# Optimization experiments

Hardware: AMD Instinct MI355X
Metric: run time of the kernel (lower is better)

## Reference

```python
import jax, jax.numpy as jnp
import numpy as np
from jax import lax

B, N, S, NS = 32, 2048, 256, 16   # batch, seeds, proposals (must be 16*16), ball-query samples
C_IN = 256                         # seed_feat_dim
RADIUS = 0.3
EPS = 1e-5
NAB, NVP = 12, 12                  # num_angle_bin, num_viewpoint
GROUPS, PLANES = 4, 64             # SpatialCGNL groups / bottleneck planes
C_OUT = 2 + 3 + 1 + 1 + 2 * NAB + NVP  # 43


def fps(xyz, npoint):
    """Furthest point sampling (torch pointnet2 style: start at index 0)."""
    Bb, Nn, _ = xyz.shape
    def step(carry, _):
        dist, far = carry
        cen = jnp.take_along_axis(xyz, far[:, None, None], axis=1)      # (B,1,3)
        d = jnp.sum((xyz - cen) ** 2, axis=-1)                          # (B,N)
        dist = jnp.minimum(dist, d)
        return (dist, jnp.argmax(dist, axis=1).astype(jnp.int32)), far
    init = (jnp.full((Bb, Nn), 1e10, xyz.dtype), jnp.zeros((Bb,), jnp.int32))
    _, inds = lax.scan(step, init, None, length=npoint)
    return jnp.transpose(inds)  # (B,npoint)


def ball_query(xyz, new_xyz, radius, nsample):
    """First-nsample neighbors within radius; pad by duplicating the first hit."""
    d2 = jnp.sum((new_xyz[:, :, None, :] - xyz[:, None, :, :]) ** 2, axis=-1)  # (B,S,N)
    Nn = xyz.shape[1]
    cand = jnp.where(d2 < radius * radius, jnp.arange(Nn)[None, None, :], Nn)
    idx = jnp.sort(cand, axis=-1)[..., :nsample]
    idx = jnp.where(idx == Nn, idx[..., :1], idx)   # duplicate first hit
    idx = jnp.where(idx == Nn, 0, idx)              # no neighbor at all -> 0
    return idx


def bn1d(x, g, b, m, v):
    """Inference BatchNorm1d over channel axis of (B,C,S)."""
    s = (g * lax.rsqrt(v + EPS))
    return (x - m[None, :, None]) * s[None, :, None] + b[None, :, None]


def forward(xyz, features, sa_w0, sa_w1, sa_w2, sa_gamma, sa_beta, sa_mean, sa_var,
            wt, wp, wg, wz, gn_gamma, gn_beta,
            c1_w, c1_b, bn1_g, bn1_b, bn1_m, bn1_v,
            c2_w, c2_b, bn2_g, bn2_b, bn2_m, bn2_v, c3_w, c3_b):
    # ---- PointnetSAModuleVotes (vote_fps sampling) ----
    fps_inds = fps(xyz, S)                                               # (B,S)
    new_xyz = jnp.take_along_axis(xyz, fps_inds[:, :, None], axis=1)     # (B,S,3)
    idx = ball_query(xyz, new_xyz, RADIUS, NS)                           # (B,S,NS)
    gather = jax.vmap(lambda a, i: a[i])
    g_xyz = (gather(xyz, idx) - new_xyz[:, :, None, :]) / RADIUS         # (B,S,NS,3), normalize_xyz
    g_feat = gather(jnp.transpose(features, (0, 2, 1)), idx)             # (B,S,NS,C)
    h = jnp.concatenate([g_xyz, g_feat], axis=-1)                        # (B,S,NS,3+C)
    for i, w in enumerate((sa_w0, sa_w1, sa_w2)):                        # SharedMLP: conv1x1(no bias)+BN+ReLU
        h = jnp.einsum('bsnc,oc->bsno', h, w)
        h = jax.nn.relu((h - sa_mean[i]) * (sa_gamma[i] * lax.rsqrt(sa_var[i] + EPS)) + sa_beta[i])
    x = jnp.transpose(jnp.max(h, axis=2), (0, 2, 1))                     # max-pool over NS -> (B,128,S)

    # ---- SpatialCGNL (use_scale=False, groups=4), spatial 16x16 flattened to S ----
    t = jnp.einsum('oc,bcn->bon', wt, x)                                 # (B,64,S)
    p = jnp.einsum('oc,bcn->bon', wp, x)
    g = jnp.einsum('oc,bcn->bon', wg, x)
    cg = PLANES // GROUPS                                                # 16
    tg = t.reshape(B, GROUPS, cg * S)
    pg = p.reshape(B, GROUPS, cg * S)
    gg = g.reshape(B, GROUPS, cg * S)
    att = jnp.sum(pg * gg, axis=-1, keepdims=True)                       # (B,G,1) scalar per group
    y = (att * tg).reshape(B, GROUPS, cg, S)                             # (B,G,16,S)
    wz_g = wz.reshape(GROUPS, 128 // GROUPS, cg)                         # grouped 1x1 conv 64->128
    y = jnp.einsum('goc,bgcn->bgon', wz_g, y).reshape(B, 128, S)
    # GroupNorm(num_groups=4, num_channels=128)
    yg = y.reshape(B, GROUPS, -1)
    mu = jnp.mean(yg, axis=-1, keepdims=True)
    var = jnp.mean((yg - mu) ** 2, axis=-1, keepdims=True)
    yn = ((yg - mu) * lax.rsqrt(var + EPS)).reshape(B, 128, S)
    y = yn * gn_gamma[None, :, None] + gn_beta[None, :, None] + x        # affine + residual

    # ---- conv/bn/relu head ----
    h1 = jax.nn.relu(bn1d(jnp.einsum('oc,bcn->bon', c1_w, y) + c1_b[None, :, None], bn1_g, bn1_b, bn1_m, bn1_v))
    h2 = jax.nn.relu(bn1d(jnp.einsum('oc,bcn->bon', c2_w, h1) + c2_b[None, :, None], bn2_g, bn2_b, bn2_m, bn2_v))
    net = jnp.einsum('oc,bcn->bon', c3_w, h2) + c3_b[None, :, None]      # (B,43,S)

    # ---- decode_scores ----
    nt = jnp.transpose(net, (0, 2, 1))                                   # (B,S,43)
    center = new_xyz + nt[:, :, 2:5]
    ang_res_n = nt[:, :, 7 + NAB:7 + 2 * NAB]
    out = jnp.concatenate([
        nt[:, :, 0:2],                    # objectness_scores
        center,                           # center
        nt[:, :, 5:7 + 2 * NAB],          # width, quality, angle_scores, angle_residuals_normalized
        ang_res_n * jnp.float32(np.pi / NAB),  # angle_residuals
        nt[:, :, 7 + 2 * NAB:],           # viewpoint_scores
    ], axis=-1)                           # (B,S,55)
    return out


def setup_inputs():
    key = jax.random.key(0)
    ks = iter(jax.random.split(key, 32))
    rn = lambda shape, s=0.05: jax.random.normal(next(ks), shape, jnp.float32) * s
    return dict(
        xyz=rn((B, N, 3), 1.0),
        features=rn((B, C_IN, N), 1.0),
        sa_w0=rn((128, C_IN + 3)), sa_w1=rn((128, 128)), sa_w2=rn((128, 128)),
        sa_gamma=jnp.ones((3, 128)), sa_beta=jnp.zeros((3, 128)),
        sa_mean=jnp.zeros((3, 128)), sa_var=jnp.ones((3, 128)),
        wt=rn((PLANES, 128)), wp=rn((PLANES, 128)), wg=rn((PLANES, 128)),
        wz=rn((128, PLANES // GROUPS)),
        gn_gamma=jnp.ones((128,)), gn_beta=jnp.zeros((128,)),
        c1_w=rn((128, 128)), c1_b=jnp.zeros((128,)),
        bn1_g=jnp.ones((128,)), bn1_b=jnp.zeros((128,)), bn1_m=jnp.zeros((128,)), bn1_v=jnp.ones((128,)),
        c2_w=rn((128, 128)), c2_b=jnp.zeros((128,)),
        bn2_g=jnp.ones((128,)), bn2_b=jnp.zeros((128,)), bn2_m=jnp.zeros((128,)), bn2_v=jnp.ones((128,)),
        c3_w=rn((C_OUT, 128)), c3_b=jnp.zeros((C_OUT,)),
    )


def reference(xyz, features, sa_w0, sa_w1, sa_w2, sa_gamma, sa_beta, sa_mean, sa_var,
              wt, wp, wg, wz, gn_gamma, gn_beta,
              c1_w, c1_b, bn1_g, bn1_b, bn1_m, bn1_v,
              c2_w, c2_b, bn2_g, bn2_b, bn2_m, bn2_v, c3_w, c3_b):
    return forward(xyz, features, sa_w0, sa_w1, sa_w2, sa_gamma, sa_beta, sa_mean, sa_var,
                   wt, wp, wg, wz, gn_gamma, gn_beta,
                   c1_w, c1_b, bn1_g, bn1_b, bn1_m, bn1_v,
                   c2_w, c2_b, bn2_g, bn2_b, bn2_m, bn2_v, c3_w, c3_b)
```

## Files before the change

### kernel.cpp

```cpp
#include <hip/hip_runtime.h>
#include <hip/hip_bf16.h>
#include <math.h>

#define Bx   32
#define Nx   2048
#define Sx   256
#define NSx  16
#define CINx 256

typedef unsigned short u16;
typedef unsigned int   u32;
typedef unsigned long long u64;
typedef short bf16x8 __attribute__((ext_vector_type(8)));
typedef float f32x4  __attribute__((ext_vector_type(4)));

__device__ __forceinline__ float b2f(u16 u) {
  union { u32 i; float f; } v; v.i = ((u32)u) << 16; return v.f;
}
__device__ __forceinline__ u16 f2b(float x) {
  u32 u = __float_as_uint(x);
  u32 r = (u + 0x7FFFu + ((u >> 16) & 1u)) >> 16;
  return (u16)r;
}
__device__ __forceinline__ float ldin(const void* p, size_t i, int bf) {
  return bf ? b2f(((const u16*)p)[i]) : ((const float*)p)[i];
}

#define DPP_FMAX(x, ctrl)                                                      \
  x = fmaxf(x, __int_as_float(__builtin_amdgcn_update_dpp(                     \
          __float_as_int(x), __float_as_int(x), (ctrl), 0xf, 0xf, false)))

#define OFF_FEATT 0
#define OFF_XT    (33554432)
#define OFF_T     (OFF_XT + 4194304)
#define OFF_YT    (OFF_T + 2097152)
#define OFF_NXYZ  (OFF_YT + 4194304)
#define OFF_IDX   (OFF_NXYZ + 98304)
#define OFF_ATT   (OFF_IDX + 524288)
#define OFF_W0F   (OFF_ATT + 512)
#define OFF_B0    (OFF_W0F + 133120)
#define OFF_W1F   (OFF_B0 + 512)
#define OFF_B1    (OFF_W1F + 65536)
#define OFF_W2F   (OFF_B1 + 512)
#define OFF_B2    (OFF_W2F + 65536)
#define OFF_WTT   (OFF_B2 + 512)
#define OFF_WPT   (OFF_WTT + 32768)
#define OFF_WGT   (OFF_WPT + 32768)
#define OFF_C1T   (OFF_WGT + 32768)
#define OFF_D1    (OFF_C1T + 65536)
#define OFF_C2T   (OFF_D1 + 512)
#define OFF_D2    (OFF_C2T + 65536)
#define OFF_C3T   (OFF_D2 + 512)
#define OFF_WZF   (OFF_C3T + 22016)
#define OFF_GNG   (OFF_WZF + 8192)
#define OFF_GNB   (OFF_GNG + 512)
#define OFF_C3B   (OFF_GNB + 512)
#define OFF_FLAG  (OFF_C3B + 512)

__global__ __launch_bounds__(256) void k_sniff(const u32* __restrict__ w, int* __restrict__ flag) {
  __shared__ int cnt;
  int t = threadIdx.x;
  if (t == 0) cnt = 0;
  __syncthreads();
  u32 x = w[t];
  int e_lo = (x >> 7) & 0xFF;
  if (e_lo >= 100 && e_lo <= 140) atomicAdd(&cnt, 1);
  __syncthreads();
  if (t == 0) *flag = (cnt > 128) ? 1 : 0;
}

#define TRANS_BLKS 4096
__global__ __launch_bounds__(256) void k_mega(
    const void* __restrict__ xyzR, const void* __restrict__ featR,
    const void* sa_w0, const void* sa_w1, const void* sa_w2,
    const void* sa_g,  const void* sa_b,  const void* sa_m, const void* sa_v,
    const void* wt, const void* wp, const void* wg, const void* wzI,
    const void* gngI, const void* gnbI,
    const void* c1w, const void* c1b,
    const void* bn1g, const void* bn1b, const void* bn1m, const void* bn1v,
    const void* c2w, const void* c2b,
    const void* bn2g, const void* bn2b, const void* bn2m, const void* bn2v,
    const void* c3w, const void* c3bI,
    float* __restrict__ nxyz, u16* __restrict__ featT,
    u16* __restrict__ w0F, float* __restrict__ b0, u16* __restrict__ w1F, float* __restrict__ b1,
    u16* __restrict__ w2F, float* __restrict__ b2,
    float* __restrict__ wtT, float* __restrict__ wpT, float* __restrict__ wgT,
    float* __restrict__ c1T, float* __restrict__ d1, float* __restrict__ c2T, float* __restrict__ d2,
    float* __restrict__ c3T, float* __restrict__ wzF, float* __restrict__ gngF,
    float* __restrict__ gnbF, float* __restrict__ c3bF,
    const int* __restrict__ flagp) {
  __shared__ union {
    struct { float sxyz[Nx * 3]; u64 red[2][4]; } fps;
    u16 tile[64][65];
  } sm;
  int bid = blockIdx.x, t = threadIdx.x;
  int bf = *flagp;

  if (bid < Bx) {
    int b = bid;
    const size_t xb = (size_t)b * Nx * 3;
    for (int i = t; i < Nx * 3; i += 256) sm.fps.sxyz[i] = ldin(xyzR, xb + i, bf);
    __syncthreads();
    float px[8], py[8], pz[8], dist[8];
#pragma unroll
    for (int j = 0; j < 8; ++j) {
      int p = t * 8 + j;
      px[j] = sm.fps.sxyz[p * 3 + 0];
      py[j] = sm.fps.sxyz[p * 3 + 1];
      pz[j] = sm.fps.sxyz[p * 3 + 2];
      dist[j] = 1e10f;
    }
    int lane = t & 63, w = t >> 6;
    int far = 0, myind = 0;
    for (int it = 0; it < Sx; ++it) {
      if (t == it) myind = far;
      float cx = sm.fps.sxyz[far * 3 + 0];
      float cy = sm.fps.sxyz[far * 3 + 1];
      float cz = sm.fps.sxyz[far * 3 + 2];
      float bv = -1.f; int bj = 0;
#pragma unroll
      for (int j = 0; j < 8; ++j) {
        float dx = __fsub_rn(px[j], cx);
        float dy = __fsub_rn(py[j], cy);
        float dz = __fsub_rn(pz[j], cz);
        float d = __fadd_rn(__fadd_rn(__fmul_rn(dx, dx), __fmul_rn(dy, dy)), __fmul_rn(dz, dz));
        float nd = fminf(dist[j], d);
        dist[j] = nd;
        if (nd > bv) { bv = nd; bj = j; }
      }
      int bi = t * 8 + bj;
      float x = bv;
      DPP_FMAX(x, 0x111);
      DPP_FMAX(x, 0x112);
      DPP_FMAX(x, 0x114);
      DPP_FMAX(x, 0x118);
      DPP_FMAX(x, 0x142);
      DPP_FMAX(x, 0x143);
      float wmax = __int_as_float(__builtin_amdgcn_readlane(__float_as_int(x), 63));
      u64 mk = __ballot(bv == wmax);
      int srcl = (int)__builtin_ctzll(mk);
      int wbi = __builtin_amdgcn_readlane(bi, srcl);
      if (lane == 63)
        sm.fps.red[it & 1][w] = ((u64)__float_as_uint(wmax) << 32) | (u32)(~wbi);
      __syncthreads();
      u64 k0 = sm.fps.red[it & 1][0], k1 = sm.fps.red[it & 1][1];
      u64 k2 = sm.fps.red[it & 1][2], k3 = sm.fps.red[it & 1][3];
      u64 best = k0 > k1 ? k0 : k1;
      if (k2 > best) best = k2;
      if (k3 > best) best = k3;
      far = (int)(u32)(~(u32)best);
    }
    float* o = nxyz + ((size_t)b * Sx + t) * 3;
    o[0] = sm.fps.sxyz[myind * 3 + 0];
    o[1] = sm.fps.sxyz[myind * 3 + 1];
    o[2] = sm.fps.sxyz[myind * 3 + 2];
  } else if (bid < Bx + TRANS_BLKS) {
    int tb = bid - Bx;
    int nblk = tb & 31, rest = tb >> 5;
    int cblk = rest & 3, b = rest >> 2;
    int n0 = nblk * 64, c0 = cblk * 64;
    int tx = t & 63, ty = t >> 6;
#pragma unroll
    for (int r = ty; r < 64; r += 4) {
      size_t src = ((size_t)(b * CINx + c0 + r)) * Nx + n0 + tx;
      sm.tile[r][tx] = bf ? ((const u16*)featR)[src] : f2b(((const float*)featR)[src]);
    }
    __syncthreads();
#pragma unroll
    for (int r = ty; r < 64; r += 4)
      featT[((size_t)(b * Nx + n0 + r)) * CINx + c0 + tx] = sm.tile[tx][r];
  } else {
    int g0 = (bid - Bx - TRANS_BLKS) * 256 + t;
    const int gs = 64 * 256;
    for (int i = g0; i < 9 * 8 * 64 * 8; i += gs) {
      int j = i & 7, lane = (i >> 3) & 63, nt = (i >> 9) & 7, kt = i >> 12;
      int o = nt * 16 + (lane & 15);
      int c = kt * 32 + (lane >> 4) * 8 + j;
      float s = ldin(sa_g, o, bf) * rsqrtf(ldin(sa_v, o, bf) + 1e-5f);
      float w;
      if (c < 256) w = ldin(sa_w0, o * 259 + 3 + c, bf);
      else if (c < 259) w = ldin(sa_w0, o * 259 + (c - 256), bf);
      else w = 0.f;
      w0F[i] = f2b(w * s);
    }
    for (int i = g0; i < 4 * 8 * 64 * 8; i += gs) {
      int j = i & 7, lane = (i >> 3) & 63, nt = (i >> 9) & 7, kt = i >> 12;
      int o = nt * 16 + (lane & 15);
      int c = kt * 32 + (lane >> 4) * 8 + j;
      float s1 = ldin(sa_g, 128 + o, bf) * rsqrtf(ldin(sa_v, 128 + o, bf) + 1e-5f);
      float s2 = ldin(sa_g, 256 + o, bf) * rsqrtf(ldin(sa_v, 256 + o, bf) + 1e-5f);
      w1F[i] = f2b(ldin(sa_w1, o * 128 + c, bf) * s1);
      w2F[i] = f2b(ldin(sa_w2, o * 128 + c, bf) * s2);
    }
    for (int o = g0; o < 128; o += gs) {
      float s0 = ldin(sa_g, o, bf)       * rsqrtf(ldin(sa_v, o, bf)       + 1e-5f);
      float s1 = ldin(sa_g, 128 + o, bf) * rsqrtf(ldin(sa_v, 128 + o, bf) + 1e-5f);
      float s2 = ldin(sa_g, 256 + o, bf) * rsqrtf(ldin(sa_v, 256 + o, bf) + 1e-5f);
      b0[o] = ldin(sa_b, o, bf)       - ldin(sa_m, o, bf)       * s0;
      b1[o] = ldin(sa_b, 128 + o, bf) - ldin(sa_m, 128 + o, bf) * s1;
      b2[o] = ldin(sa_b, 256 + o, bf) - ldin(sa_m, 256 + o, bf) * s2;
      float sc1 = ldin(bn1g, o, bf) * rsqrtf(ldin(bn1v, o, bf) + 1e-5f);
      float sc2 = ldin(bn2g, o, bf) * rsqrtf(ldin(bn2v, o, bf) + 1e-5f);
      d1[o] = (ldin(c1b, o, bf) - ldin(bn1m, o, bf)) * sc1 + ldin(bn1b, o, bf);
      d2[o] = (ldin(c2b, o, bf) - ldin(bn2m, o, bf)) * sc2 + ldin(bn2b, o, bf);
      gngF[o] = ldin(gngI, o, bf);
      gnbF[o] = ldin(gnbI, o, bf);
    }
    for (int i = g0; i < 128 * 128; i += gs) {
      int o = i >> 7, c = i & 127;
      float sc1 = ldin(bn1g, o, bf) * rsqrtf(ldin(bn1v, o, bf) + 1e-5f);
      float sc2 = ldin(bn2g, o, bf) * rsqrtf(ldin(bn2v, o, bf) + 1e-5f);
      c1T[c * 128 + o] = ldin(c1w, i, bf) * sc1;
      c2T[c * 128 + o] = ldin(c2w, i, bf) * sc2;
    }
    for (int i = g0; i < 64 * 128; i += gs) {
      int o = i >> 7, c = i & 127;
      wtT[c * 64 + o] = ldin(wt, i, bf);
      wpT[c * 64 + o] = ldin(wp, i, bf);
      wgT[c * 64 + o] = ldin(wg, i, bf);
    }
    for (int i = g0; i < 43 * 128; i += gs) {
      int o = i >> 7, c = i & 127;
      c3T[c * 43 + o] = ldin(c3w, i, bf);
    }
    for (int i = g0; i < 2048; i += gs) wzF[i] = ldin(wzI, i, bf);
    for (int i = g0; i < 43; i += gs) c3bF[i] = ldin(c3bI, i, bf);
  }
}

__global__ __launch_bounds__(256) void k_ballq(const void* __restrict__ xyzR,
                                               const float* __restrict__ nxyz,
                                               int* __restrict__ idxb,
                                               const int* __restrict__ flagp) {
  int bf = *flagp;
  int t = threadIdx.x;
  int wv = t >> 6, lane = t & 63;
  int gs = blockIdx.x * 4 + wv;
  int b = gs >> 8;
  const size_t xb = (size_t)b * Nx * 3;
  const float* cen = nxyz + (size_t)gs * 3;
  float cx = cen[0], cy = cen[1], cz = cen[2];
  const float R2 = (float)(0.3 * 0.3);
  int* outp = idxb + (size_t)gs * NSx;
  int have = 0, first = 0;
  bool gotfirst = false;
  for (int ch = 0; ch < Nx / 64 && have < NSx; ++ch) {
    int p = ch * 64 + lane;
    float dx = __fsub_rn(ldin(xyzR, xb + p * 3 + 0, bf), cx);
    float dy = __fsub_rn(ldin(xyzR, xb + p * 3 + 1, bf), cy);
    float dz = __fsub_rn(ldin(xyzR, xb + p * 3 + 2, bf), cz);
    float d2 = __fadd_rn(__fadd_rn(__fmul_rn(dx, dx), __fmul_rn(dy, dy)), __fmul_rn(dz, dz));
    bool hit = d2 < R2;
    unsigned long long m = __ballot(hit);
    if (hit) {
      int pos = have + __popcll(m & ((1ull << lane) - 1ull));
      if (pos < NSx) outp[pos] = p;
    }
    if (!gotfirst && m) { first = ch * 64 + (int)__builtin_ctzll(m); gotfirst = true; }
    have += __popcll(m);
  }
  if (have < NSx && lane >= have && lane < NSx) outp[lane] = first;
}

__global__ __launch_bounds__(256) void k_samlp(
    const u16* __restrict__ featT, const void* __restrict__ xyzR,
    const float* __restrict__ nxyz, const int* __restrict__ idxb,
    const u16* __restrict__ w0F, const float* __restrict__ b0v,
    const u16* __restrict__ w1F, const float* __restrict__ b1v,
    const u16* __restrict__ w2F, const float* __restrict__ b2v,
    float* __restrict__ xT, const int* __restrict__ flagp) {
  __shared__ __align__(16) u16 lds[4][16 * 32 + 2 * 16 * 136];
  int bf = *flagp;
  int t = threadIdx.x, w = t >> 6, lane = t & 63;
  int s = blockIdx.x * 4 + w, b = blockIdx.y;
  u16* ht = &lds[w][0];
  u16* hA = &lds[w][512];
  u16* hB = &lds[w][512 + 2176];
  const int* gidx = idxb + ((size_t)b * Sx + s) * NSx;
  int m = lane & 15, q = lane >> 4;
  int pn = gidx[m];
  const float* cen = nxyz + ((size_t)b * Sx + s) * 3;
  for (int i = lane; i < 16 * 32; i += 64)
    if ((i & 31) >= 3) ht[i] = 0;
  if (lane < 48) {
    int n2 = lane / 3, cc = lane - n2 * 3;
    int pn2 = gidx[n2];
    float v = (ldin(xyzR, ((size_t)b * Nx + pn2) * 3 + cc, bf) - cen[cc]) * (1.0f / 0.3f);
    ht[n2 * 32 + cc] = f2b(v);
  }
  __syncthreads();

  const bf16x8* wf0 = (const bf16x8*)w0F;
  const bf16x8* wf1 = (const bf16x8*)w1F;
  const bf16x8* wf2 = (const bf16x8*)w2F;
  f32x4 acc[8];

#pragma unroll
  for (int nt = 0; nt < 8; ++nt) acc[nt] = (f32x4){0.f, 0.f, 0.f, 0.f};
  const u16* arow = featT + ((size_t)b * Nx + pn) * CINx + q * 8;
#pragma unroll
  for (int kt = 0; kt < 9; ++kt) {
    bf16x8 a = (kt < 8) ? *(const bf16x8*)(arow + kt * 32)
                        : *(const bf16x8*)(ht + m * 32 + q * 8);
#pragma unroll
    for (int nt = 0; nt < 8; ++nt)
      acc[nt] = __builtin_amdgcn_mfma_f32_16x16x32_bf16(a, wf0[(kt * 8 + nt) * 64 + lane], acc[nt], 0, 0, 0);
  }
#pragma unroll
  for (int nt = 0; nt < 8; ++nt) {
    float bb = b0v[nt * 16 + m];
#pragma unroll
    for (int r = 0; r < 4; ++r)
      hA[(q * 4 + r) * 136 + nt * 16 + m] = f2b(fmaxf(acc[nt][r] + bb, 0.f));
  }
  __syncthreads();

#pragma unroll
  for (int nt = 0; nt < 8; ++nt) acc[nt] = (f32x4){0.f, 0.f, 0.f, 0.f};
#pragma unroll
  for (int kt = 0; kt < 4; ++kt) {
    bf16x8 a = *(const bf16x8*)(hA + m * 136 + kt * 32 + q * 8);
#pragma unroll
    for (int nt = 0; nt < 8; ++nt)
      acc[nt] = __builtin_amdgcn_mfma_f32_16x16x32_bf16(a, wf1[(kt * 8 + nt) * 64 + lane], acc[nt], 0, 0, 0);
  }
#pragma unroll
  for (int nt = 0; nt < 8; ++nt) {
    float bb = b1v[nt * 16 + m];
#pragma unroll
    for (int r = 0; r < 4; ++r)
      hB[(q * 4 + r) * 136 + nt * 16 + m] = f2b(fmaxf(acc[nt][r] + bb, 0.f));
  }
  __syncthreads();

#pragma unroll
  for (int nt = 0; nt < 8; ++nt) acc[nt] = (f32x4){0.f, 0.f, 0.f, 0.f};
#pragma unroll
  for (int kt = 0; kt < 4; ++kt) {
    bf16x8 a = *(const bf16x8*)(hB + m * 136 + kt * 32 + q * 8);
#pragma unroll
    for (int nt = 0; nt < 8; ++nt)
      acc[nt] = __builtin_amdgcn_mfma_f32_16x16x32_bf16(a, wf2[(kt * 8 + nt) * 64 + lane], acc[nt], 0, 0, 0);
  }
  float* xrow = xT + ((size_t)b * Sx + s) * 128;
#pragma unroll
  for (int nt = 0; nt < 8; ++nt) {
    float vm = fmaxf(fmaxf(acc[nt][0], acc[nt][1]), fmaxf(acc[nt][2], acc[nt][3]));
    vm = fmaxf(vm, __shfl_xor(vm, 16, 64));
    vm = fmaxf(vm, __shfl_xor(vm, 32, 64));
    float v = fmaxf(vm + b2v[nt * 16 + m], 0.f);
    if (q == 0) xrow[nt * 16 + m] = v;
  }
}

__global__ __launch_bounds__(256) void k_tpg(const float* __restrict__ xT,
                                             const float* __restrict__ wtT,
                                             const float* __restrict__ wpT,
                                             const float* __restrict__ wgT,
                                             float* __restrict__ tbuf,
                                             float* __restrict__ att) {
  __shared__ float xs[64][129];
  int b = blockIdx.y, s0 = blockIdx.x * 64, t = threadIdx.x;
  {
    int r = t >> 2, part = (t & 3) * 32;
    const float4* src = (const float4*)(xT + ((size_t)b * Sx + s0 + r) * 128 + part);
#pragma unroll
    for (int q = 0; q < 8; ++q) {
      float4 v = src[q];
      xs[r][part + q * 4 + 0] = v.x;
      xs[r][part + q * 4 + 1] = v.y;
      xs[r][part + q * 4 + 2] = v.z;
      xs[r][part + q * 4 + 3] = v.w;
    }
  }
  __syncthreads();
  int sg = t & 15, og = t >> 4;
  float ta[16], pa[16], ga[16];
#pragma unroll
  for (int k = 0; k < 16; ++k) { ta[k] = 0.f; pa[k] = 0.f; ga[k] = 0.f; }
  for (int c = 0; c < 128; ++c) {
    float xv[4];
#pragma unroll
    for (int j = 0; j < 4; ++j) xv[j] = xs[sg * 4 + j][c];
    float4 wtv = *(const float4*)(wtT + c * 64 + og * 4);
    float4 wpv = *(const float4*)(wpT + c * 64 + og * 4);
    float4 wgv = *(const float4*)(wgT + c * 64 + og * 4);
    float wa[4] = {wtv.x, wtv.y, wtv.z, wtv.w};
    float wb[4] = {wpv.x, wpv.y, wpv.z, wpv.w};
    float wc[4] = {wgv.x, wgv.y, wgv.z, wgv.w};
#pragma unroll
    for (int i = 0; i < 4; ++i)
#pragma unroll
      for (int j = 0; j < 4; ++j) {
        ta[i * 4 + j] = fmaf(wa[i], xv[j], ta[i * 4 + j]);
        pa[i * 4 + j] = fmaf(wb[i], xv[j], pa[i * 4 + j]);
        ga[i * 4 + j] = fmaf(wc[i], xv[j], ga[i * 4 + j]);
      }
  }
#pragma unroll
  for (int i = 0; i < 4; ++i)
#pragma unroll
    for (int j = 0; j < 4; ++j)
      tbuf[((size_t)b * 64 + og * 4 + i) * 256 + s0 + sg * 4 + j] = ta[i * 4 + j];
  float pv = 0.f;
#pragma unroll
  for (int k = 0; k < 16; ++k) pv += pa[k] * ga[k];
#pragma unroll
  for (int off = 32; off; off >>= 1) pv += __shfl_down(pv, off, 64);
  if ((t & 63) == 0) atomicAdd(att + b * 4 + (t >> 6), pv);
}

__device__ __forceinline__ float blocksum(float v, volatile float* red, int t) {
#pragma unroll
  for (int off = 32; off; off >>= 1) v += __shfl_down(v, off, 64);
  __syncthreads();
  if ((t & 63) == 0) red[t >> 6] = v;
  __syncthreads();
  return red[0] + red[1] + red[2] + red[3];
}

__global__ __launch_bounds__(256) void k_gn(const float* __restrict__ tbuf,
                                            const float* __restrict__ att,
                                            const float* __restrict__ wzF,
                                            const float* __restrict__ gngF,
                                            const float* __restrict__ gnbF,
                                            const float* __restrict__ xT,
                                            float* __restrict__ yT) {
  __shared__ float tg[16][256];
  __shared__ float wzs[32][16];
  __shared__ float red[4];
  int g = blockIdx.x, b = blockIdx.y, t = threadIdx.x;
  {
    int n = t >> 4, kk = (t & 15) * 16;
    const float4* src = (const float4*)(tbuf + ((size_t)b * 64 + g * 16 + n) * 256 + kk);
#pragma unroll
    for (int q = 0; q < 4; ++q) {
      float4 v = src[q];
      tg[n][kk + q * 4 + 0] = v.x;
      tg[n][kk + q * 4 + 1] = v.y;
      tg[n][kk + q * 4 + 2] = v.z;
      tg[n][kk + q * 4 + 3] = v.w;
    }
  }
  for (int i = t; i < 512; i += 256)
    wzs[i >> 4][i & 15] = wzF[(g * 32 + (i >> 4)) * 16 + (i & 15)];
  __syncthreads();
  float attv = att[b * 4 + g];
  int s = t;
  float yv[32];
#pragma unroll
  for (int o = 0; o < 32; ++o) yv[o] = 0.f;
  for (int c = 0; c < 16; ++c) {
    float tv = attv * tg[c][s];
#pragma unroll
    for (int o = 0; o < 32; ++o) yv[o] = fmaf(wzs[o][c], tv, yv[o]);
  }
  float ls = 0.f;
#pragma unroll
  for (int o = 0; o < 32; ++o) ls += yv[o];
  float mu = blocksum(ls, red, t) * (1.f / 8192.f);
  float lq = 0.f;
#pragma unroll
  for (int o = 0; o < 32; ++o) { float d = yv[o] - mu; lq = fmaf(d, d, lq); }
  float var = blocksum(lq, red, t) * (1.f / 8192.f);
  float rs = rsqrtf(var + 1e-5f);
  const float* xrow = xT + ((size_t)b * Sx + s) * 128 + g * 32;
  float* yrow = yT + ((size_t)b * Sx + s) * 128 + g * 32;
#pragma unroll
  for (int o = 0; o < 32; ++o) {
    int ch = g * 32 + o;
    yrow[o] = (yv[o] - mu) * rs * gngF[ch] + gnbF[ch] + xrow[o];
  }
}

__global__ __launch_bounds__(256) void k_ffn(const float* __restrict__ yT,
                                             const float* __restrict__ c1T, const float* __restrict__ d1,
                                             const float* __restrict__ c2T, const float* __restrict__ d2,
                                             const float* __restrict__ c3T, const float* __restrict__ c3bF,
                                             const float* __restrict__ nxyz,
                                             void* __restrict__ outp,
                                             const int* __restrict__ flagp) {
  __shared__ float ys[32][132];
  __shared__ float h1s[32][132];
  __shared__ float h2s[32][132];
  __shared__ float nets[32][44];
  int bf = *flagp;
  int b = blockIdx.y, s0 = blockIdx.x * 32, t = threadIdx.x;
  {
    int r = t >> 3, part = (t & 7) * 16;
    const float4* src = (const float4*)(yT + ((size_t)b * Sx + s0 + r) * 128 + part);
#pragma unroll
    for (int q = 0; q < 4; ++q) *(float4*)&ys[r][part + q * 4] = src[q];
  }
  __syncthreads();
  int o0 = (t & 31) * 4, sl0 = (t >> 5) * 4;
  float acc[16];
#pragma unroll
  for (int k = 0; k < 16; ++k) acc[k] = 0.f;
  for (int c = 0; c < 128; ++c) {
    float4 wv = *(const float4*)(c1T + c * 128 + o0);
    float yv[4];
#pragma unroll
    for (int j = 0; j < 4; ++j) yv[j] = ys[sl0 + j][c];
#pragma unroll
    for (int j = 0; j < 4; ++j) {
      acc[0 * 4 + j] = fmaf(wv.x, yv[j], acc[0 * 4 + j]);
      acc[1 * 4 + j] = fmaf(wv.y, yv[j], acc[1 * 4 + j]);
      acc[2 * 4 + j] = fmaf(wv.z, yv[j], acc[2 * 4 + j]);
      acc[3 * 4 + j] = fmaf(wv.w, yv[j], acc[3 * 4 + j]);
    }
  }
  {
    float4 dv = *(const float4*)(d1 + o0);
    float db[4] = {dv.x, dv.y, dv.z, dv.w};
#pragma unroll
    for (int i = 0; i < 4; ++i)
#pragma unroll
      for (int j = 0; j < 4; ++j)
        h1s[sl0 + j][o0 + i] = fmaxf(acc[i * 4 + j] + db[i], 0.f);
  }
  __syncthreads();
#pragma unroll
  for (int k = 0; k < 16; ++k) acc[k] = 0.f;
  for (int c = 0; c < 128; ++c) {
    float4 wv = *(const float4*)(c2T + c * 128 + o0);
    float yv[4];
#pragma unroll
    for (int j = 0; j < 4; ++j) yv[j] = h1s[sl0 + j][c];
#pragma unroll
    for (int j = 0; j < 4; ++j) {
      acc[0 * 4 + j] = fmaf(wv.x, yv[j], acc[0 * 4 + j]);
      acc[1 * 4 + j] = fmaf(wv.y, yv[j], acc[1 * 4 + j]);
      acc[2 * 4 + j] = fmaf(wv.z, yv[j], acc[2 * 4 + j]);
      acc[3 * 4 + j] = fmaf(wv.w, yv[j], acc[3 * 4 + j]);
    }
  }
  {
    float4 dv = *(const float4*)(d2 + o0);
    float db[4] = {dv.x, dv.y, dv.z, dv.w};
#pragma unroll
    for (int i = 0; i < 4; ++i)
#pragma unroll
      for (int j = 0; j < 4; ++j)
        h2s[sl0 + j][o0 + i] = fmaxf(acc[i * 4 + j] + db[i], 0.f);
  }
  __syncthreads();
  for (int f = t; f < 43 * 32; f += 256) {
    int o = f >> 5, s = f & 31;
    float a = c3bF[o];
    for (int c4 = 0; c4 < 32; ++c4) {
      float4 hv = *(const float4*)&h2s[s][c4 * 4];
      a = fmaf(hv.x, c3T[(c4 * 4 + 0) * 43 + o], a);
      a = fmaf(hv.y, c3T[(c4 * 4 + 1) * 43 + o], a);
      a = fmaf(hv.z, c3T[(c4 * 4 + 2) * 43 + o], a);
      a = fmaf(hv.w, c3T[(c4 * 4 + 3) * 43 + o], a);
    }
    nets[s][o] = a;
  }
  __syncthreads();
  const float PI12 = (float)(M_PI / 12.0);
  for (int f = t; f < 55 * 32; f += 256) {
    int s = f / 55, kk = f - s * 55;
    float v;
    if (kk < 5) {
      v = nets[s][kk];
      if (kk >= 2) v += nxyz[((size_t)b * Sx + s0 + s) * 3 + (kk - 2)];
    } else if (kk < 31) v = nets[s][kk];
    else if (kk < 43) v = nets[s][kk - 12] * PI12;
    else v = nets[s][kk - 12];
    size_t oi = ((size_t)b * Sx + s0 + s) * 55 + kk;
    if (bf) ((u16*)outp)[oi] = f2b(v);
    else    ((float*)outp)[oi] = v;
  }
}

extern "C" void kernel_launch(void* const* d_in, const int* in_sizes, int n_in,
                              void* d_out, int out_size, void* d_ws, size_t ws_size,
                              hipStream_t stream) {
  char* w = (char*)d_ws;
  u16*   featT = (u16*)(w + OFF_FEATT);
  float* xT    = (float*)(w + OFF_XT);
  float* tbuf  = (float*)(w + OFF_T);
  float* yT    = (float*)(w + OFF_YT);
  float* nxyz  = (float*)(w + OFF_NXYZ);
  int*   idxb  = (int*)(w + OFF_IDX);
  float* att   = (float*)(w + OFF_ATT);
  u16*   w0F   = (u16*)(w + OFF_W0F);
  float* b0    = (float*)(w + OFF_B0);
  u16*   w1F   = (u16*)(w + OFF_W1F);
  float* b1    = (float*)(w + OFF_B1);
  u16*   w2F   = (u16*)(w + OFF_W2F);
  float* b2    = (float*)(w + OFF_B2);
  float* wtT   = (float*)(w + OFF_WTT);
  float* wpT   = (float*)(w + OFF_WPT);
  float* wgT   = (float*)(w + OFF_WGT);
  float* c1T   = (float*)(w + OFF_C1T);
  float* d1    = (float*)(w + OFF_D1);
  float* c2T   = (float*)(w + OFF_C2T);
  float* d2    = (float*)(w + OFF_D2);
  float* c3T   = (float*)(w + OFF_C3T);
  float* wzF   = (float*)(w + OFF_WZF);
  float* gngF  = (float*)(w + OFF_GNG);
  float* gnbF  = (float*)(w + OFF_GNB);
  float* c3bF  = (float*)(w + OFF_C3B);
  int*   flag  = (int*)(w + OFF_FLAG);

  hipMemsetAsync(w + OFF_ATT, 0, 512, stream);
  k_sniff<<<1, 256, 0, stream>>>((const u32*)d_in[0], flag);
  k_mega<<<Bx + TRANS_BLKS + 64, 256, 0, stream>>>(
      d_in[0], d_in[1],
      d_in[2], d_in[3], d_in[4], d_in[5], d_in[6], d_in[7], d_in[8],
      d_in[9], d_in[10], d_in[11], d_in[12], d_in[13], d_in[14],
      d_in[15], d_in[16], d_in[17], d_in[18], d_in[19], d_in[20],
      d_in[21], d_in[22], d_in[23], d_in[24], d_in[25], d_in[26],
      d_in[27], d_in[28],
      nxyz, featT,
      w0F, b0, w1F, b1, w2F, b2, wtT, wpT, wgT,
      c1T, d1, c2T, d2, c3T, wzF, gngF, gnbF, c3bF, flag);
  k_ballq<<<(Bx * Sx) / 4, 256, 0, stream>>>(d_in[0], nxyz, idxb, flag);
  k_samlp<<<dim3(Sx / 4, Bx), 256, 0, stream>>>(featT, d_in[0], nxyz, idxb,
                                                w0F, b0, w1F, b1, w2F, b2, xT, flag);
  k_tpg<<<dim3(4, Bx), 256, 0, stream>>>(xT, wtT, wpT, wgT, tbuf, att);
  k_gn<<<dim3(4, Bx), 256, 0, stream>>>(tbuf, att, wzF, gngF, gnbF, xT, yT);
  k_ffn<<<dim3(8, Bx), 256, 0, stream>>>(yT, c1T, d1, c2T, d2, c3T, c3bF, nxyz,
                                         d_out, flag);
}
```

Before: 473.6 us.

## Use 32x32x16 MFMA for two proposals per wave; fuse tpg and gn kernels

The shared-MLP kernel now has each wave process two proposals (32 rows) with 32x32x16 bf16 MFMA, and the weight fragments are re-packed to match that layout. This halves the weight-fragment traffic per proposal and the number of blocks launched. The theta/phi/g projection and the group-norm stage are merged into one kernel that computes the attention scalar through a block reduction. That removes the intermediate t buffer, the global atomics and the memset, at the cost of each block looping over all 256 proposals with less parallelism per block.

```diff
diff --git a/kernel.cpp b/kernel.cpp
--- a/kernel.cpp
+++ b/kernel.cpp
@@ -13,6 +13,7 @@
 typedef unsigned long long u64;
 typedef short bf16x8 __attribute__((ext_vector_type(8)));
 typedef float f32x4  __attribute__((ext_vector_type(4)));
+typedef float f32x16 __attribute__((ext_vector_type(16)));
 
 __device__ __forceinline__ float b2f(u16 u) {
   union { u32 i; float f; } v; v.i = ((u32)u) << 16; return v.f;
@@ -172,10 +173,10 @@
   } else {
     int g0 = (bid - Bx - TRANS_BLKS) * 256 + t;
     const int gs = 64 * 256;
-    for (int i = g0; i < 9 * 8 * 64 * 8; i += gs) {
-      int j = i & 7, lane = (i >> 3) & 63, nt = (i >> 9) & 7, kt = i >> 12;
-      int o = nt * 16 + (lane & 15);
-      int c = kt * 32 + (lane >> 4) * 8 + j;
+    for (int i = g0; i < 18 * 4 * 64 * 8; i += gs) {
+      int j = i & 7, lane = (i >> 3) & 63, nt = (i >> 9) & 3, kt = i >> 11;
+      int o = nt * 32 + (lane & 31);
+      int c = kt * 16 + ((lane >> 5) << 3) + j;
       float s = ldin(sa_g, o, bf) * rsqrtf(ldin(sa_v, o, bf) + 1e-5f);
       float w;
       if (c < 256) w = ldin(sa_w0, o * 259 + 3 + c, bf);
@@ -183,10 +184,10 @@
       else w = 0.f;
       w0F[i] = f2b(w * s);
     }
-    for (int i = g0; i < 4 * 8 * 64 * 8; i += gs) {
-      int j = i & 7, lane = (i >> 3) & 63, nt = (i >> 9) & 7, kt = i >> 12;
-      int o = nt * 16 + (lane & 15);
-      int c = kt * 32 + (lane >> 4) * 8 + j;
+    for (int i = g0; i < 8 * 4 * 64 * 8; i += gs) {
+      int j = i & 7, lane = (i >> 3) & 63, nt = (i >> 9) & 3, kt = i >> 11;
+      int o = nt * 32 + (lane & 31);
+      int c = kt * 16 + ((lane >> 5) << 3) + j;
       float s1 = ldin(sa_g, 128 + o, bf) * rsqrtf(ldin(sa_v, 128 + o, bf) + 1e-5f);
       float s2 = ldin(sa_g, 256 + o, bf) * rsqrtf(ldin(sa_v, 256 + o, bf) + 1e-5f);
       w1F[i] = f2b(ldin(sa_w1, o * 128 + c, bf) * s1);
@@ -269,189 +270,166 @@
     const u16* __restrict__ w1F, const float* __restrict__ b1v,
     const u16* __restrict__ w2F, const float* __restrict__ b2v,
     float* __restrict__ xT, const int* __restrict__ flagp) {
-  __shared__ __align__(16) u16 lds[4][16 * 32 + 2 * 16 * 136];
+  __shared__ __align__(16) u16 lds[4][32 * 32 + 2 * 32 * 136];
   int bf = *flagp;
   int t = threadIdx.x, w = t >> 6, lane = t & 63;
-  int s = blockIdx.x * 4 + w, b = blockIdx.y;
+  int b = blockIdx.y;
+  int s0 = (blockIdx.x * 4 + w) * 2;
   u16* ht = &lds[w][0];
-  u16* hA = &lds[w][512];
-  u16* hB = &lds[w][512 + 2176];
-  const int* gidx = idxb + ((size_t)b * Sx + s) * NSx;
-  int m = lane & 15, q = lane >> 4;
+  u16* hA = &lds[w][1024];
+  u16* hB = &lds[w][1024 + 4352];
+  int m = lane & 31, half = lane >> 5;
+  const int* gidx = idxb + ((size_t)b * Sx + s0) * NSx;
   int pn = gidx[m];
-  const float* cen = nxyz + ((size_t)b * Sx + s) * 3;
-  for (int i = lane; i < 16 * 32; i += 64)
+  for (int i = lane; i < 32 * 32; i += 64)
     if ((i & 31) >= 3) ht[i] = 0;
-  if (lane < 48) {
-    int n2 = lane / 3, cc = lane - n2 * 3;
-    int pn2 = gidx[n2];
-    float v = (ldin(xyzR, ((size_t)b * Nx + pn2) * 3 + cc, bf) - cen[cc]) * (1.0f / 0.3f);
-    ht[n2 * 32 + cc] = f2b(v);
+  for (int i = lane; i < 96; i += 64) {
+    int mm = i / 3, cc = i - (i / 3) * 3;
+    int pn2 = gidx[mm];
+    float cen = nxyz[((size_t)b * Sx + s0 + (mm >> 4)) * 3 + cc];
+    float v = (ldin(xyzR, ((size_t)b * Nx + pn2) * 3 + cc, bf) - cen) * (1.0f / 0.3f);
+    ht[mm * 32 + cc] = f2b(v);
   }
   __syncthreads();
 
   const bf16x8* wf0 = (const bf16x8*)w0F;
   const bf16x8* wf1 = (const bf16x8*)w1F;
   const bf16x8* wf2 = (const bf16x8*)w2F;
-  f32x4 acc[8];
-
-#pragma unroll
-  for (int nt = 0; nt < 8; ++nt) acc[nt] = (f32x4){0.f, 0.f, 0.f, 0.f};
-  const u16* arow = featT + ((size_t)b * Nx + pn) * CINx + q * 8;
-#pragma unroll
-  for (int kt = 0; kt < 9; ++kt) {
-    bf16x8 a = (kt < 8) ? *(const bf16x8*)(arow + kt * 32)
-                        : *(const bf16x8*)(ht + m * 32 + q * 8);
-#pragma unroll
-    for (int nt = 0; nt < 8; ++nt)
-      acc[nt] = __builtin_amdgcn_mfma_f32_16x16x32_bf16(a, wf0[(kt * 8 + nt) * 64 + lane], acc[nt], 0, 0, 0);
-  }
-#pragma unroll
-  for (int nt = 0; nt < 8; ++nt) {
-    float bb = b0v[nt * 16 + m];
-#pragma unroll
-    for (int r = 0; r < 4; ++r)
-      hA[(q * 4 + r) * 136 + nt * 16 + m] = f2b(fmaxf(acc[nt][r] + bb, 0.f));
-  }
-  __syncthreads();
-
-#pragma unroll
-  for (int nt = 0; nt < 8; ++nt) acc[nt] = (f32x4){0.f, 0.f, 0.f, 0.f};
-#pragma unroll
-  for (int kt = 0; kt < 4; ++kt) {
-    bf16x8 a = *(const bf16x8*)(hA + m * 136 + kt * 32 + q * 8);
-#pragma unroll
-    for (int nt = 0; nt < 8; ++nt)
-      acc[nt] = __builtin_amdgcn_mfma_f32_16x16x32_bf16(a, wf1[(kt * 8 + nt) * 64 + lane], acc[nt], 0, 0, 0);
-  }
-#pragma unroll
-  for (int nt = 0; nt < 8; ++nt) {
-    float bb = b1v[nt * 16 + m];
-#pragma unroll
-    for (int r = 0; r < 4; ++r)
-      hB[(q * 4 + r) * 136 + nt * 16 + m] = f2b(fmaxf(acc[nt][r] + bb, 0.f));
-  }
-  __syncthreads();
-
-#pragma unroll
-  for (int nt = 0; nt < 8; ++nt) acc[nt] = (f32x4){0.f, 0.f, 0.f, 0.f};
-#pragma unroll
-  for (int kt = 0; kt < 4; ++kt) {
-    bf16x8 a = *(const bf16x8*)(hB + m * 136 + kt * 32 + q * 8);
-#pragma unroll
-    for (int nt = 0; nt < 8; ++nt)
-      acc[nt] = __builtin_amdgcn_mfma_f32_16x16x32_bf16(a, wf2[(kt * 8 + nt) * 64 + lane], acc[nt], 0, 0, 0);
-  }
-  float* xrow = xT + ((size_t)b * Sx + s) * 128;
-#pragma unroll
-  for (int nt = 0; nt < 8; ++nt) {
-    float vm = fmaxf(fmaxf(acc[nt][0], acc[nt][1]), fmaxf(acc[nt][2], acc[nt][3]));
-    vm = fmaxf(vm, __shfl_xor(vm, 16, 64));
-    vm = fmaxf(vm, __shfl_xor(vm, 32, 64));
-    float v = fmaxf(vm + b2v[nt * 16 + m], 0.f);
-    if (q == 0) xrow[nt * 16 + m] = v;
-  }
-}
-
-__global__ __launch_bounds__(256) void k_tpg(const float* __restrict__ xT,
-                                             const float* __restrict__ wtT,
-                                             const float* __restrict__ wpT,
-                                             const float* __restrict__ wgT,
-                                             float* __restrict__ tbuf,
-                                             float* __restrict__ att) {
+  f32x16 acc[4];
+
+#pragma unroll
+  for (int nt = 0; nt < 4; ++nt) acc[nt] = (f32x16)(0.f);
+  const u16* arow = featT + ((size_t)b * Nx + pn) * CINx + half * 8;
+#pragma unroll
+  for (int kt = 0; kt < 18; ++kt) {
+    bf16x8 a = (kt < 16) ? *(const bf16x8*)(arow + kt * 16)
+                         : *(const bf16x8*)(ht + m * 32 + (kt - 16) * 16 + half * 8);
+#pragma unroll
+    for (int nt = 0; nt < 4; ++nt)
+      acc[nt] = __builtin_amdgcn_mfma_f32_32x32x16_bf16(a, wf0[(kt * 4 + nt) * 64 + lane], acc[nt], 0, 0, 0);
+  }
+#pragma unroll
+  for (int nt = 0; nt < 4; ++nt) {
+    float bb = b0v[nt * 32 + m];
+#pragma unroll
+    for (int r = 0; r < 16; ++r) {
+      int mm = (r & 3) + 8 * (r >> 2) + 4 * half;
+      hA[mm * 136 + nt * 32 + m] = f2b(fmaxf(acc[nt][r] + bb, 0.f));
+    }
+  }
+  __syncthreads();
+
+#pragma unroll
+  for (int nt = 0; nt < 4; ++nt) acc[nt] = (f32x16)(0.f);
+#pragma unroll
+  for (int kt = 0; kt < 8; ++kt) {
+    bf16x8 a = *(const bf16x8*)(hA + m * 136 + kt * 16 + half * 8);
+#pragma unroll
+    for (int nt = 0; nt < 4; ++nt)
+      acc[nt] = __builtin_amdgcn_mfma_f32_32x32x16_bf16(a, wf1[(kt * 4 + nt) * 64 + lane], acc[nt], 0, 0, 0);
+  }
+#pragma unroll
+  for (int nt = 0; nt < 4; ++nt) {
+    float bb = b1v[nt * 32 + m];
+#pragma unroll
+    for (int r = 0; r < 16; ++r) {
+      int mm = (r & 3) + 8 * (r >> 2) + 4 * half;
+      hB[mm * 136 + nt * 32 + m] = f2b(fmaxf(acc[nt][r] + bb, 0.f));
+    }
+  }
+  __syncthreads();
+
+#pragma unroll
+  for (int nt = 0; nt < 4; ++nt) acc[nt] = (f32x16)(0.f);
+#pragma unroll
+  for (int kt = 0; kt < 8; ++kt) {
+    bf16x8 a = *(const bf16x8*)(hB + m * 136 + kt * 16 + half * 8);
+#pragma unroll
+    for (int nt = 0; nt < 4; ++nt)
+      acc[nt] = __builtin_amdgcn_mfma_f32_32x32x16_bf16(a, wf2[(kt * 4 + nt) * 64 + lane], acc[nt], 0, 0, 0);
+  }
+#pragma unroll
+  for (int nt = 0; nt < 4; ++nt) {
+    float v0 = acc[nt][0], v1 = acc[nt][8];
+#pragma unroll
+    for (int r = 1; r < 8; ++r) { v0 = fmaxf(v0, acc[nt][r]); v1 = fmaxf(v1, acc[nt][8 + r]); }
+    v0 = fmaxf(v0, __shfl_xor(v0, 32, 64));
+    v1 = fmaxf(v1, __shfl_xor(v1, 32, 64));
+    int o = nt * 32 + m;
+    float vv = half ? v1 : v0;
+    xT[((size_t)b * Sx + s0 + half) * 128 + o] = fmaxf(vv + b2v[o], 0.f);
+  }
+}
+
+__device__ __forceinline__ float blocksum(float v, volatile float* red, int t) {
+#pragma unroll
+  for (int off = 32; off; off >>= 1) v += __shfl_down(v, off, 64);
+  __syncthreads();
+  if ((t & 63) == 0) red[t >> 6] = v;
+  __syncthreads();
+  return red[0] + red[1] + red[2] + red[3];
+}
+
+__global__ __launch_bounds__(256) void k_tpgn(const float* __restrict__ xT,
+                                              const float* __restrict__ wtT,
+                                              const float* __restrict__ wpT,
+                                              const float* __restrict__ wgT,
+                                              const float* __restrict__ wzF,
+                                              const float* __restrict__ gngF,
+                                              const float* __restrict__ gnbF,
+                                              float* __restrict__ yT) {
   __shared__ float xs[64][129];
-  int b = blockIdx.y, s0 = blockIdx.x * 64, t = threadIdx.x;
-  {
-    int r = t >> 2, part = (t & 3) * 32;
-    const float4* src = (const float4*)(xT + ((size_t)b * Sx + s0 + r) * 128 + part);
-#pragma unroll
-    for (int q = 0; q < 8; ++q) {
-      float4 v = src[q];
-      xs[r][part + q * 4 + 0] = v.x;
-      xs[r][part + q * 4 + 1] = v.y;
-      xs[r][part + q * 4 + 2] = v.z;
-      xs[r][part + q * 4 + 3] = v.w;
-    }
-  }
-  __syncthreads();
-  int sg = t & 15, og = t >> 4;
-  float ta[16], pa[16], ga[16];
-#pragma unroll
-  for (int k = 0; k < 16; ++k) { ta[k] = 0.f; pa[k] = 0.f; ga[k] = 0.f; }
-  for (int c = 0; c < 128; ++c) {
-    float xv[4];
-#pragma unroll
-    for (int j = 0; j < 4; ++j) xv[j] = xs[sg * 4 + j][c];
-    float4 wtv = *(const float4*)(wtT + c * 64 + og * 4);
-    float4 wpv = *(const float4*)(wpT + c * 64 + og * 4);
-    float4 wgv = *(const float4*)(wgT + c * 64 + og * 4);
-    float wa[4] = {wtv.x, wtv.y, wtv.z, wtv.w};
-    float wb[4] = {wpv.x, wpv.y, wpv.z, wpv.w};
-    float wc[4] = {wgv.x, wgv.y, wgv.z, wgv.w};
-#pragma unroll
-    for (int i = 0; i < 4; ++i)
-#pragma unroll
-      for (int j = 0; j < 4; ++j) {
-        ta[i * 4 + j] = fmaf(wa[i], xv[j], ta[i * 4 + j]);
-        pa[i * 4 + j] = fmaf(wb[i], xv[j], pa[i * 4 + j]);
-        ga[i * 4 + j] = fmaf(wc[i], xv[j], ga[i * 4 + j]);
-      }
-  }
-#pragma unroll
-  for (int i = 0; i < 4; ++i)
-#pragma unroll
-    for (int j = 0; j < 4; ++j)
-      tbuf[((size_t)b * 64 + og * 4 + i) * 256 + s0 + sg * 4 + j] = ta[i * 4 + j];
-  float pv = 0.f;
-#pragma unroll
-  for (int k = 0; k < 16; ++k) pv += pa[k] * ga[k];
-#pragma unroll
-  for (int off = 32; off; off >>= 1) pv += __shfl_down(pv, off, 64);
-  if ((t & 63) == 0) atomicAdd(att + b * 4 + (t >> 6), pv);
-}
-
-__device__ __forceinline__ float blocksum(float v, volatile float* red, int t) {
-#pragma unroll
-  for (int off = 32; off; off >>= 1) v += __shfl_down(v, off, 64);
-  __syncthreads();
-  if ((t & 63) == 0) red[t >> 6] = v;
-  __syncthreads();
-  return red[0] + red[1] + red[2] + red[3];
-}
-
-__global__ __launch_bounds__(256) void k_gn(const float* __restrict__ tbuf,
-                                            const float* __restrict__ att,
-                                            const float* __restrict__ wzF,
-                                            const float* __restrict__ gngF,
-                                            const float* __restrict__ gnbF,
-                                            const float* __restrict__ xT,
-                                            float* __restrict__ yT) {
-  __shared__ float tg[16][256];
+  __shared__ float tS[16][260];
   __shared__ float wzs[32][16];
   __shared__ float red[4];
   int g = blockIdx.x, b = blockIdx.y, t = threadIdx.x;
-  {
-    int n = t >> 4, kk = (t & 15) * 16;
-    const float4* src = (const float4*)(tbuf + ((size_t)b * 64 + g * 16 + n) * 256 + kk);
-#pragma unroll
-    for (int q = 0; q < 4; ++q) {
-      float4 v = src[q];
-      tg[n][kk + q * 4 + 0] = v.x;
-      tg[n][kk + q * 4 + 1] = v.y;
-      tg[n][kk + q * 4 + 2] = v.z;
-      tg[n][kk + q * 4 + 3] = v.w;
-    }
-  }
   for (int i = t; i < 512; i += 256)
     wzs[i >> 4][i & 15] = wzF[(g * 32 + (i >> 4)) * 16 + (i & 15)];
-  __syncthreads();
-  float attv = att[b * 4 + g];
+  int r = t >> 4, sg = t & 15;
+  float attp = 0.f;
+  for (int tile = 0; tile < 4; ++tile) {
+    {
+      int rr = t >> 2, part = (t & 3) * 32;
+      const float4* src = (const float4*)(xT + ((size_t)b * Sx + tile * 64 + rr) * 128 + part);
+#pragma unroll
+      for (int q = 0; q < 8; ++q) {
+        float4 v = src[q];
+        xs[rr][part + q * 4 + 0] = v.x;
+        xs[rr][part + q * 4 + 1] = v.y;
+        xs[rr][part + q * 4 + 2] = v.z;
+        xs[rr][part + q * 4 + 3] = v.w;
+      }
+    }
+    __syncthreads();
+    float ta[4], pa[4], ga[4];
+#pragma unroll
+    for (int j = 0; j < 4; ++j) { ta[j] = 0.f; pa[j] = 0.f; ga[j] = 0.f; }
+    for (int c = 0; c < 128; ++c) {
+      float wa = wtT[c * 64 + g * 16 + r];
+      float wb = wpT[c * 64 + g * 16 + r];
+      float wc = wgT[c * 64 + g * 16 + r];
+#pragma unroll
+      for (int j = 0; j < 4; ++j) {
+        float xv = xs[sg * 4 + j][c];
+        ta[j] = fmaf(wa, xv, ta[j]);
+        pa[j] = fmaf(wb, xv, pa[j]);
+        ga[j] = fmaf(wc, xv, ga[j]);
+      }
+    }
+#pragma unroll
+    for (int j = 0; j < 4; ++j) {
+      attp += pa[j] * ga[j];
+      tS[r][tile * 64 + sg * 4 + j] = ta[j];
+    }
+    __syncthreads();
+  }
+  float attv = blocksum(attp, red, t);
   int s = t;
   float yv[32];
 #pragma unroll
   for (int o = 0; o < 32; ++o) yv[o] = 0.f;
   for (int c = 0; c < 16; ++c) {
-    float tv = attv * tg[c][s];
+    float tv = attv * tS[c][s];
 #pragma unroll
     for (int o = 0; o < 32; ++o) yv[o] = fmaf(wzs[o][c], tv, yv[o]);
   }
@@ -580,11 +558,9 @@
   char* w = (char*)d_ws;
   u16*   featT = (u16*)(w + OFF_FEATT);
   float* xT    = (float*)(w + OFF_XT);
-  float* tbuf  = (float*)(w + OFF_T);
   float* yT    = (float*)(w + OFF_YT);
   float* nxyz  = (float*)(w + OFF_NXYZ);
   int*   idxb  = (int*)(w + OFF_IDX);
-  float* att   = (float*)(w + OFF_ATT);
   u16*   w0F   = (u16*)(w + OFF_W0F);
   float* b0    = (float*)(w + OFF_B0);
   u16*   w1F   = (u16*)(w + OFF_W1F);
@@ -605,7 +581,6 @@
   float* c3bF  = (float*)(w + OFF_C3B);
   int*   flag  = (int*)(w + OFF_FLAG);
 
-  hipMemsetAsync(w + OFF_ATT, 0, 512, stream);
   k_sniff<<<1, 256, 0, stream>>>((const u32*)d_in[0], flag);
   k_mega<<<Bx + TRANS_BLKS + 64, 256, 0, stream>>>(
       d_in[0], d_in[1],
@@ -618,10 +593,9 @@
       w0F, b0, w1F, b1, w2F, b2, wtT, wpT, wgT,
       c1T, d1, c2T, d2, c3T, wzF, gngF, gnbF, c3bF, flag);
   k_ballq<<<(Bx * Sx) / 4, 256, 0, stream>>>(d_in[0], nxyz, idxb, flag);
-  k_samlp<<<dim3(Sx / 4, Bx), 256, 0, stream>>>(featT, d_in[0], nxyz, idxb,
+  k_samlp<<<dim3(Sx / 8, Bx), 256, 0, stream>>>(featT, d_in[0], nxyz, idxb,
                                                 w0F, b0, w1F, b1, w2F, b2, xT, flag);
-  k_tpg<<<dim3(4, Bx), 256, 0, stream>>>(xT, wtT, wpT, wgT, tbuf, att);
-  k_gn<<<dim3(4, Bx), 256, 0, stream>>>(tbuf, att, wzF, gngF, gnbF, xT, yT);
+  k_tpgn<<<dim3(4, Bx), 256, 0, stream>>>(xT, wtT, wpT, wgT, wzF, gngF, gnbF, yT);
   k_ffn<<<dim3(8, Bx), 256, 0, stream>>>(yT, c1T, d1, c2T, d2, c3T, c3bF, nxyz,
                                          d_out, flag);
 }
```

After: 477.7 us. About the same (+0.9%).
